# Kernel tuning notes

Hardware: AMD Instinct MI355X
Metric: run time of the kernel (lower is better)

## Reference

```python
import jax, jax.numpy as jnp
import numpy as np

EMBED = 1024

def setup_inputs() -> dict:
    key = jax.random.key(0)
    ks = jax.random.split(key, 10)
    B, S, E = 4, 2048, EMBED
    inv = 1.0 / np.sqrt(E)
    return {
        "query": jax.random.normal(ks[0], (B, S, E), jnp.float32),
        "key": jax.random.normal(ks[1], (B, S, E), jnp.float32),
        "value": jax.random.normal(ks[2], (B, S, E), jnp.float32),
        "attn_mask": jnp.zeros((B, S, S), jnp.float32),
        "Wq": jax.random.normal(ks[3], (E, E), jnp.float32) * inv,
        "bq": jnp.zeros((E,), jnp.float32),
        "Wk": jax.random.normal(ks[4], (E, E), jnp.float32) * inv,
        "bk": jnp.zeros((E,), jnp.float32),
        "Wv": jax.random.normal(ks[5], (E, E), jnp.float32) * inv,
        "bv": jnp.zeros((E,), jnp.float32),
    }

def reference(query, key, value, attn_mask, Wq, bq, Wk, bk, Wv, bv):
    E = query.shape[-1]
    q = query @ Wq.T + bq            # [B,S,E]
    k = key @ Wk.T + bk              # [B,S,E]
    v = value @ Wv.T + bv            # [B,S,E]
    scores = jnp.einsum('bse,bte->bst', q, k) / jnp.sqrt(jnp.float32(E))
    scores = scores + attn_mask      # [B,S,S]
    attn = jax.nn.softmax(scores, axis=-1)
    return jnp.einsum('bst,bte->bse', attn, v)
```

## Files before the change

kernel.cpp:

```cpp
#include <hip/hip_runtime.h>
#include <cstdint>
#include <cstddef>

typedef __bf16 bf16;
typedef __bf16 bf16x8 __attribute__((ext_vector_type(8)));
typedef float  f32x4  __attribute__((ext_vector_type(4)));

#define NB 4
#define SS 2048
#define EE 1024

#define BUFB      49152
#define LDS_TOTAL (3 * BUFB)

static __device__ __forceinline__ void glds16(const bf16* g, void* l)
{
    __builtin_amdgcn_global_load_lds(
        (const __attribute__((address_space(1))) unsigned int*)g,
        (__attribute__((address_space(3))) unsigned int*)l,
        16, 0, 0);
}

static __device__ __forceinline__ void swz_block(int& bx, int& by, int& bz)
{
    const int nx = gridDim.x, ny = gridDim.y;
    const int nwg = nx * ny * gridDim.z;
    int lin = blockIdx.x + nx * (blockIdx.y + ny * blockIdx.z);
    const int per = nwg >> 3;
    lin = (lin & 7) * per + (lin >> 3);
    bz = lin / (nx * ny);
    const int r = lin - bz * nx * ny;
    by = r / nx;
    bx = r - by * nx;
}

static __device__ __forceinline__ void kloop(
    const bf16* __restrict__ A, const bf16* __restrict__ Bm,
    int lda, int ldb, int nt, char* lds, int m0, int n0, int tid,
    f32x4 acc[4][4])
{
    const int lane = tid & 63, w = tid >> 6;
    const int wm = w >> 2, wn = w & 3;
    const int lr = lane & 15, kq = lane >> 4;
    const int axor = (lr & 7) << 4;

    const int srow   = tid >> 3;
    const int chunkL = (tid & 7) ^ (srow & 7);
    const bf16* Asrc = A  + (size_t)(m0 + srow) * lda + chunkL * 8;
    const bf16* Bsrc = Bm + (size_t)(n0 + srow) * ldb + chunkL * 8;
    const int wofs = w << 10;

#pragma unroll
    for (int p = 0; p < 2; ++p) {
        char* d = lds + p * BUFB + wofs;
        const int kt = p * 64;
        glds16(Asrc + kt,                        d);
        glds16(Asrc + (size_t)64 * lda + kt,     d + 8192);
        glds16(Bsrc + kt,                        d + 16384);
        glds16(Bsrc + (size_t)64 * ldb + kt,     d + 16384 + 8192);
        glds16(Bsrc + (size_t)128 * ldb + kt,    d + 16384 + 16384);
        glds16(Bsrc + (size_t)192 * ldb + kt,    d + 16384 + 24576);
    }
    asm volatile("s_waitcnt vmcnt(6)" ::: "memory");
    __builtin_amdgcn_sched_barrier(0);
    __builtin_amdgcn_s_barrier();
    __builtin_amdgcn_sched_barrier(0);

    for (int t = 0; t < nt; ++t) {
        char* la = lds + (t % 3) * BUFB;
        char* lb = la + 16384;
        char* sa = lds + ((t + 2) % 3) * BUFB;
        const bool st = (t + 2) < nt;
        const int kt = (t + 2) * 64;

        bf16x8 af[4], bg[4];
        {
            const int cb = (kq * 16) ^ axor;
#pragma unroll
            for (int m = 0; m < 4; ++m)
                af[m] = *(const bf16x8*)(la + (wm * 64 + m * 16 + lr) * 128 + cb);
#pragma unroll
            for (int n = 0; n < 4; ++n)
                bg[n] = *(const bf16x8*)(lb + (wn * 64 + n * 16 + lr) * 128 + cb);
            if (st) {
                glds16(Asrc + kt,                    sa + wofs);
                glds16(Asrc + (size_t)64 * lda + kt, sa + 8192 + wofs);
                glds16(Bsrc + kt,                    sa + 16384 + wofs);
            }
            __builtin_amdgcn_s_setprio(1);
#pragma unroll
            for (int m = 0; m < 4; ++m)
#pragma unroll
                for (int n = 0; n < 4; ++n)
                    acc[m][n] = __builtin_amdgcn_mfma_f32_16x16x32_bf16(af[m], bg[n], acc[m][n], 0, 0, 0);
            __builtin_amdgcn_s_setprio(0);
        }
        {
            const int cb = (64 + kq * 16) ^ axor;
#pragma unroll
            for (int m = 0; m < 4; ++m)
                af[m] = *(const bf16x8*)(la + (wm * 64 + m * 16 + lr) * 128 + cb);
#pragma unroll
            for (int n = 0; n < 4; ++n)
                bg[n] = *(const bf16x8*)(lb + (wn * 64 + n * 16 + lr) * 128 + cb);
            if (st) {
                glds16(Bsrc + (size_t)64 * ldb + kt,  sa + 16384 + 8192 + wofs);
                glds16(Bsrc + (size_t)128 * ldb + kt, sa + 16384 + 16384 + wofs);
                glds16(Bsrc + (size_t)192 * ldb + kt, sa + 16384 + 24576 + wofs);
            }
            __builtin_amdgcn_s_setprio(1);
#pragma unroll
            for (int m = 0; m < 4; ++m)
#pragma unroll
                for (int n = 0; n < 4; ++n)
                    acc[m][n] = __builtin_amdgcn_mfma_f32_16x16x32_bf16(af[m], bg[n], acc[m][n], 0, 0, 0);
            __builtin_amdgcn_s_setprio(0);
        }
        if (t < nt - 1) {
            if (st) { asm volatile("s_waitcnt vmcnt(6)" ::: "memory"); }
            else    { asm volatile("s_waitcnt vmcnt(0)" ::: "memory"); }
            __builtin_amdgcn_sched_barrier(0);
            __builtin_amdgcn_s_barrier();
            __builtin_amdgcn_sched_barrier(0);
        }
    }
}

__global__ __launch_bounds__(256) void cvt3_kernel(
    const float* __restrict__ s0, const float* __restrict__ s1, const float* __restrict__ s2,
    bf16* __restrict__ d0, bf16* __restrict__ d1, bf16* __restrict__ d2, unsigned n)
{
    const float* s; bf16* d;
    if (blockIdx.y == 0)      { s = s0; d = d0; }
    else if (blockIdx.y == 1) { s = s1; d = d1; }
    else                      { s = s2; d = d2; }
    const size_t i = ((size_t)blockIdx.x * 256 + threadIdx.x) * 8;
    if (i >= n) return;
    const float4 f0 = *(const float4*)(s + i);
    const float4 f1 = *(const float4*)(s + i + 4);
    bf16x8 h;
    h[0] = (bf16)f0.x; h[1] = (bf16)f0.y; h[2] = (bf16)f0.z; h[3] = (bf16)f0.w;
    h[4] = (bf16)f1.x; h[5] = (bf16)f1.y; h[6] = (bf16)f1.z; h[7] = (bf16)f1.w;
    *(bf16x8*)(d + i) = h;
}

__global__ __launch_bounds__(512) void proj8(
    const bf16* __restrict__ qc, const bf16* __restrict__ kc, const bf16* __restrict__ vc,
    const bf16* __restrict__ Wc,
    const float* __restrict__ bq, const float* __restrict__ bk, const float* __restrict__ bv,
    bf16* __restrict__ qb, bf16* __restrict__ kb, bf16* __restrict__ vb)
{
    extern __shared__ char lds[];
    int bx, by, bz; swz_block(bx, by, bz);
    const bf16* A; const float* bias; bf16* out;
    if (bz == 0)      { A = qc; bias = bq; out = qb; }
    else if (bz == 1) { A = kc; bias = bk; out = kb; }
    else              { A = vc; bias = bv; out = vb; }
    const bf16* Bm = Wc + (size_t)bz * EE * EE;

    const int m0 = by * 128, n0 = bx * 256;
    const int tid = threadIdx.x;

    f32x4 acc[4][4];
#pragma unroll
    for (int m = 0; m < 4; ++m)
#pragma unroll
        for (int n = 0; n < 4; ++n) { acc[m][n][0] = 0.f; acc[m][n][1] = 0.f; acc[m][n][2] = 0.f; acc[m][n][3] = 0.f; }

    kloop(A, Bm, EE, EE, EE / 64, lds, m0, n0, tid, acc);

    const int lane = tid & 63, w = tid >> 6, wm = w >> 2, wn = w & 3;
    const int lr = lane & 15, kq = lane >> 4;
#pragma unroll
    for (int n = 0; n < 4; ++n) {
        const int gcol = n0 + wn * 64 + n * 16 + lr;
        const float bb = bias[gcol];
#pragma unroll
        for (int m = 0; m < 4; ++m)
#pragma unroll
            for (int j = 0; j < 4; ++j) {
                const int grow = m0 + wm * 64 + m * 16 + kq * 4 + j;
                out[(size_t)grow * EE + gcol] = (bf16)(acc[m][n][j] + bb);
            }
    }
}

__global__ __launch_bounds__(256) void transpose_kernel(const bf16* __restrict__ vb,
                                                        bf16* __restrict__ vt)
{
    __shared__ bf16 t[64][72];
    const int b  = blockIdx.z;
    const int s0 = blockIdx.x * 64, e0 = blockIdx.y * 64;
    const int tid = threadIdx.x;

    const bf16* src = vb + ((size_t)b * SS + s0) * EE + e0;
#pragma unroll
    for (int i = 0; i < 2; ++i) {
        const int c  = tid * 2 + i;
        const int r  = c >> 3;
        const int cc = (c & 7) * 8;
        *(uint4*)&t[r][cc] = *(const uint4*)&src[(size_t)r * EE + cc];
    }
    __syncthreads();

    bf16* dst = vt + ((size_t)b * EE + e0) * SS + s0;
    const int er  = tid >> 2;
    const int sc0 = (tid & 3) * 16;
    bf16 tmp[16];
#pragma unroll
    for (int k2 = 0; k2 < 16; ++k2) tmp[k2] = t[sc0 + k2][er];
    *(uint4*)&dst[(size_t)er * SS + sc0]     = *(uint4*)&tmp[0];
    *(uint4*)&dst[(size_t)er * SS + sc0 + 8] = *(uint4*)&tmp[8];
}

__global__ __launch_bounds__(512) void scores8(const bf16* __restrict__ qb,
                                               const bf16* __restrict__ kb,
                                               const float* __restrict__ mask,
                                               bf16* __restrict__ sc)
{
    extern __shared__ char lds[];
    int bx, by, bz; swz_block(bx, by, bz);
    const bf16* A  = qb + (size_t)bz * SS * EE;
    const bf16* Bm = kb + (size_t)bz * SS * EE;

    const int m0 = by * 128, n0 = bx * 256;
    const int tid = threadIdx.x;

    f32x4 acc[4][4];
#pragma unroll
    for (int m = 0; m < 4; ++m)
#pragma unroll
        for (int n = 0; n < 4; ++n) { acc[m][n][0] = 0.f; acc[m][n][1] = 0.f; acc[m][n][2] = 0.f; acc[m][n][3] = 0.f; }

    kloop(A, Bm, EE, EE, EE / 64, lds, m0, n0, tid, acc);

    const int lane = tid & 63, w = tid >> 6, wm = w >> 2, wn = w & 3;
    const int lr = lane & 15, kq = lane >> 4;
    const float* mrow = mask + (size_t)bz * SS * SS;
    bf16* out = sc + (size_t)bz * SS * SS;
    const float scale = 0.03125f;
#pragma unroll
    for (int m = 0; m < 4; ++m)
#pragma unroll
        for (int n = 0; n < 4; ++n)
#pragma unroll
            for (int j = 0; j < 4; ++j) {
                const int grow = m0 + wm * 64 + m * 16 + kq * 4 + j;
                const int gcol = n0 + wn * 64 + n * 16 + lr;
                const float v = acc[m][n][j] * scale + mrow[(size_t)grow * SS + gcol];
                out[(size_t)grow * SS + gcol] = (bf16)v;
            }
}

__global__ __launch_bounds__(256) void softmax_kernel(bf16* __restrict__ sc)
{
    __shared__ float red[4];
    const size_t row = blockIdx.x;
    uint4* rp = (uint4*)(sc + row * (size_t)SS);
    const int tid = threadIdx.x, lane = tid & 63, wid = tid >> 6;

    const uint4 d = rp[tid];
    const unsigned int u[4] = { d.x, d.y, d.z, d.w };
    float f[8];
#pragma unroll
    for (int i = 0; i < 4; ++i) {
        union { unsigned int i_; float f_; } lo, hi;
        lo.i_ = u[i] << 16;
        hi.i_ = u[i] & 0xffff0000u;
        f[2 * i]     = lo.f_;
        f[2 * i + 1] = hi.f_;
    }

    float m = f[0];
#pragma unroll
    for (int i = 1; i < 8; ++i) m = fmaxf(m, f[i]);
#pragma unroll
    for (int o = 32; o > 0; o >>= 1) m = fmaxf(m, __shfl_xor(m, o));
    if (lane == 0) red[wid] = m;
    __syncthreads();
    m = fmaxf(fmaxf(red[0], red[1]), fmaxf(red[2], red[3]));
    __syncthreads();

    float e[8], s = 0.f;
#pragma unroll
    for (int i = 0; i < 8; ++i) { e[i] = __expf(f[i] - m); s += e[i]; }
#pragma unroll
    for (int o = 32; o > 0; o >>= 1) s += __shfl_xor(s, o);
    if (lane == 0) red[wid] = s;
    __syncthreads();
    s = red[0] + red[1] + red[2] + red[3];
    const float inv = 1.0f / s;

    unsigned int ou[4];
#pragma unroll
    for (int i = 0; i < 4; ++i) {
        union { bf16 h; unsigned short b; } a0, a1;
        a0.h = (bf16)(e[2 * i] * inv);
        a1.h = (bf16)(e[2 * i + 1] * inv);
        ou[i] = ((unsigned int)a1.b << 16) | (unsigned int)a0.b;
    }
    rp[tid] = make_uint4(ou[0], ou[1], ou[2], ou[3]);
}

__global__ __launch_bounds__(512) void pv8(const bf16* __restrict__ sc,
                                           const bf16* __restrict__ vt,
                                           float* __restrict__ outp)
{
    extern __shared__ char lds[];
    int bx, by, bz; swz_block(bx, by, bz);
    const bf16* A  = sc + (size_t)bz * SS * SS;
    const bf16* Bm = vt + (size_t)bz * EE * SS;

    const int m0 = by * 128, n0 = bx * 256;
    const int tid = threadIdx.x;

    f32x4 acc[4][4];
#pragma unroll
    for (int m = 0; m < 4; ++m)
#pragma unroll
        for (int n = 0; n < 4; ++n) { acc[m][n][0] = 0.f; acc[m][n][1] = 0.f; acc[m][n][2] = 0.f; acc[m][n][3] = 0.f; }

    kloop(A, Bm, SS, SS, SS / 64, lds, m0, n0, tid, acc);

    const int lane = tid & 63, w = tid >> 6, wm = w >> 2, wn = w & 3;
    const int lr = lane & 15, kq = lane >> 4;
#pragma unroll
    for (int m = 0; m < 4; ++m)
#pragma unroll
        for (int n = 0; n < 4; ++n)
#pragma unroll
            for (int j = 0; j < 4; ++j) {
                const int grow = m0 + wm * 64 + m * 16 + kq * 4 + j;
                const int gcol = n0 + wn * 64 + n * 16 + lr;
                outp[((size_t)bz * SS + grow) * EE + gcol] = acc[m][n][j];
            }
}

extern "C" void kernel_launch(void* const* d_in, const int* in_sizes, int n_in,
                              void* d_out, int out_size, void* d_ws, size_t ws_size,
                              hipStream_t stream)
{
    const float* query = (const float*)d_in[0];
    const float* key_  = (const float*)d_in[1];
    const float* value = (const float*)d_in[2];
    const float* mask  = (const float*)d_in[3];
    const float* Wq = (const float*)d_in[4];
    const float* bq = (const float*)d_in[5];
    const float* Wk = (const float*)d_in[6];
    const float* bk = (const float*)d_in[7];
    const float* Wv = (const float*)d_in[8];
    const float* bv = (const float*)d_in[9];
    float* outp = (float*)d_out;

    char* ws = (char*)d_ws;
    const size_t QKV = (size_t)NB * SS * EE * 2;
    const size_t SCB = (size_t)NB * SS * SS * 2;
    const size_t WCB = (size_t)3 * EE * EE * 2;
    if (ws_size < 4 * QKV + SCB + WCB) return;

    bf16* qb = (bf16*)(ws);
    bf16* kb = (bf16*)(ws + QKV);
    bf16* vb = (bf16*)(ws + 2 * QKV);
    bf16* vt = (bf16*)(ws + 3 * QKV);
    bf16* sc = (bf16*)(ws + 4 * QKV);
    bf16* Wc = (bf16*)(ws + 4 * QKV + SCB);
    bf16* qc = vt;
    bf16* kc = sc;
    bf16* vc = (bf16*)(ws + 5 * QKV);

    (void)hipFuncSetAttribute((const void*)proj8,   hipFuncAttributeMaxDynamicSharedMemorySize, LDS_TOTAL);
    (void)hipFuncSetAttribute((const void*)scores8, hipFuncAttributeMaxDynamicSharedMemorySize, LDS_TOTAL);
    (void)hipFuncSetAttribute((const void*)pv8,     hipFuncAttributeMaxDynamicSharedMemorySize, LDS_TOTAL);

    dim3 blk(256), blk5(512);
    const unsigned NQKV = (unsigned)NB * SS * EE;
    const unsigned NW   = (unsigned)EE * EE;
    cvt3_kernel<<<dim3(NQKV / (256 * 8), 3), blk, 0, stream>>>(
        query, key_, value, qc, kc, vc, NQKV);
    cvt3_kernel<<<dim3(NW / (256 * 8), 3), blk, 0, stream>>>(
        Wq, Wk, Wv, Wc, Wc + (size_t)EE * EE, Wc + 2 * (size_t)EE * EE, NW);

    proj8<<<dim3(EE / 256, (NB * SS) / 128, 3), blk5, LDS_TOTAL, stream>>>(
        qc, kc, vc, Wc, bq, bk, bv, qb, kb, vb);
    transpose_kernel<<<dim3(SS / 64, EE / 64, NB), blk, 0, stream>>>(vb, vt);
    scores8<<<dim3(SS / 256, SS / 128, NB), blk5, LDS_TOTAL, stream>>>(qb, kb, mask, sc);
    softmax_kernel<<<dim3(NB * SS), blk, 0, stream>>>(sc);
    pv8<<<dim3(EE / 256, SS / 128, NB), blk5, LDS_TOTAL, stream>>>(sc, vt, outp);
}
```

Before: 196.0 us.

## Halve GEMM K-tile to 32 and deepen LDS pipeline for higher occupancy

The shared GEMM main loop now stages K in steps of 32 instead of 64, using a 24KB per-stage LDS buffer with a 4-chunk XOR swizzle. Projection and scores kernels keep 3 stages and request 4 workgroups per CU. The PV kernel uses a 6-stage ring for deeper prefetch and requests 2 workgroups per CU. The aim is more resident waves and more loads in flight to hide memory latency, at the cost of twice as many barriers per K and possible register pressure from the launch bounds.

```diff
diff --git a/kernel.cpp b/kernel.cpp
--- a/kernel.cpp
+++ b/kernel.cpp
@@ -10,8 +10,9 @@
 #define SS 2048
 #define EE 1024
 
-#define BUFB      49152
-#define LDS_TOTAL (3 * BUFB)
+#define BUFB  24576
+#define LDS3  (3 * BUFB)
+#define LDS6  (6 * BUFB)
 
 static __device__ __forceinline__ void glds16(const bf16* g, void* l)
 {
@@ -34,7 +35,8 @@
     bx = r - by * nx;
 }
 
-static __device__ __forceinline__ void kloop(
+template<int NBUF>
+static __device__ __forceinline__ void kloop32(
     const bf16* __restrict__ A, const bf16* __restrict__ Bm,
     int lda, int ldb, int nt, char* lds, int m0, int n0, int tid,
     f32x4 acc[4][4])
@@ -42,88 +44,67 @@
     const int lane = tid & 63, w = tid >> 6;
     const int wm = w >> 2, wn = w & 3;
     const int lr = lane & 15, kq = lane >> 4;
-    const int axor = (lr & 7) << 4;
-
-    const int srow   = tid >> 3;
-    const int chunkL = (tid & 7) ^ (srow & 7);
+    const int cb = (kq * 16) ^ ((lr & 3) << 4);
+
+    const int srow   = tid >> 2;
+    const int chunkL = (tid & 3) ^ (srow & 3);
     const bf16* Asrc = A  + (size_t)(m0 + srow) * lda + chunkL * 8;
     const bf16* Bsrc = Bm + (size_t)(n0 + srow) * ldb + chunkL * 8;
     const int wofs = w << 10;
 
 #pragma unroll
-    for (int p = 0; p < 2; ++p) {
+    for (int p = 0; p < NBUF - 1; ++p) {
         char* d = lds + p * BUFB + wofs;
-        const int kt = p * 64;
-        glds16(Asrc + kt,                        d);
-        glds16(Asrc + (size_t)64 * lda + kt,     d + 8192);
-        glds16(Bsrc + kt,                        d + 16384);
-        glds16(Bsrc + (size_t)64 * ldb + kt,     d + 16384 + 8192);
-        glds16(Bsrc + (size_t)128 * ldb + kt,    d + 16384 + 16384);
-        glds16(Bsrc + (size_t)192 * ldb + kt,    d + 16384 + 24576);
-    }
-    asm volatile("s_waitcnt vmcnt(6)" ::: "memory");
+        const int kt = p * 32;
+        glds16(Asrc + kt,                     d);
+        glds16(Bsrc + kt,                     d + 8192);
+        glds16(Bsrc + (size_t)128 * ldb + kt, d + 16384);
+    }
+    if constexpr (NBUF == 3) asm volatile("s_waitcnt vmcnt(3)" ::: "memory");
+    else                     asm volatile("s_waitcnt vmcnt(12)" ::: "memory");
     __builtin_amdgcn_sched_barrier(0);
     __builtin_amdgcn_s_barrier();
     __builtin_amdgcn_sched_barrier(0);
 
+    int rb = 0, sb = NBUF - 1;
     for (int t = 0; t < nt; ++t) {
-        char* la = lds + (t % 3) * BUFB;
-        char* lb = la + 16384;
-        char* sa = lds + ((t + 2) % 3) * BUFB;
-        const bool st = (t + 2) < nt;
-        const int kt = (t + 2) * 64;
+        char* la = lds + rb * BUFB;
+        char* lb = la + 8192;
+        const int ts = (t + NBUF - 1 < nt) ? t + NBUF - 1 : nt - 1;
+        const int kt = ts * 32;
+        char* d = lds + sb * BUFB + wofs;
 
         bf16x8 af[4], bg[4];
-        {
-            const int cb = (kq * 16) ^ axor;
-#pragma unroll
-            for (int m = 0; m < 4; ++m)
-                af[m] = *(const bf16x8*)(la + (wm * 64 + m * 16 + lr) * 128 + cb);
+#pragma unroll
+        for (int m = 0; m < 4; ++m)
+            af[m] = *(const bf16x8*)(la + (wm * 64 + m * 16 + lr) * 64 + cb);
+#pragma unroll
+        for (int n = 0; n < 4; ++n)
+            bg[n] = *(const bf16x8*)(lb + (wn * 64 + n * 16 + lr) * 64 + cb);
+
+        glds16(Asrc + kt,                     d);
+        glds16(Bsrc + kt,                     d + 8192);
+        glds16(Bsrc + (size_t)128 * ldb + kt, d + 16384);
+
+        __builtin_amdgcn_s_setprio(1);
+#pragma unroll
+        for (int m = 0; m < 4; ++m)
 #pragma unroll
             for (int n = 0; n < 4; ++n)
-                bg[n] = *(const bf16x8*)(lb + (wn * 64 + n * 16 + lr) * 128 + cb);
-            if (st) {
-                glds16(Asrc + kt,                    sa + wofs);
-                glds16(Asrc + (size_t)64 * lda + kt, sa + 8192 + wofs);
-                glds16(Bsrc + kt,                    sa + 16384 + wofs);
-            }
-            __builtin_amdgcn_s_setprio(1);
-#pragma unroll
-            for (int m = 0; m < 4; ++m)
-#pragma unroll
-                for (int n = 0; n < 4; ++n)
-                    acc[m][n] = __builtin_amdgcn_mfma_f32_16x16x32_bf16(af[m], bg[n], acc[m][n], 0, 0, 0);
-            __builtin_amdgcn_s_setprio(0);
-        }
-        {
-            const int cb = (64 + kq * 16) ^ axor;
-#pragma unroll
-            for (int m = 0; m < 4; ++m)
-                af[m] = *(const bf16x8*)(la + (wm * 64 + m * 16 + lr) * 128 + cb);
-#pragma unroll
-            for (int n = 0; n < 4; ++n)
-                bg[n] = *(const bf16x8*)(lb + (wn * 64 + n * 16 + lr) * 128 + cb);
-            if (st) {
-                glds16(Bsrc + (size_t)64 * ldb + kt,  sa + 16384 + 8192 + wofs);
-                glds16(Bsrc + (size_t)128 * ldb + kt, sa + 16384 + 16384 + wofs);
-                glds16(Bsrc + (size_t)192 * ldb + kt, sa + 16384 + 24576 + wofs);
-            }
-            __builtin_amdgcn_s_setprio(1);
-#pragma unroll
-            for (int m = 0; m < 4; ++m)
-#pragma unroll
-                for (int n = 0; n < 4; ++n)
-                    acc[m][n] = __builtin_amdgcn_mfma_f32_16x16x32_bf16(af[m], bg[n], acc[m][n], 0, 0, 0);
-            __builtin_amdgcn_s_setprio(0);
-        }
+                acc[m][n] = __builtin_amdgcn_mfma_f32_16x16x32_bf16(af[m], bg[n], acc[m][n], 0, 0, 0);
+        __builtin_amdgcn_s_setprio(0);
+
         if (t < nt - 1) {
-            if (st) { asm volatile("s_waitcnt vmcnt(6)" ::: "memory"); }
-            else    { asm volatile("s_waitcnt vmcnt(0)" ::: "memory"); }
+            if constexpr (NBUF == 3) asm volatile("s_waitcnt vmcnt(3)" ::: "memory");
+            else                     asm volatile("s_waitcnt vmcnt(12)" ::: "memory");
             __builtin_amdgcn_sched_barrier(0);
             __builtin_amdgcn_s_barrier();
             __builtin_amdgcn_sched_barrier(0);
         }
-    }
+        rb = (rb + 1 == NBUF) ? 0 : rb + 1;
+        sb = (sb + 1 == NBUF) ? 0 : sb + 1;
+    }
+    asm volatile("s_waitcnt vmcnt(0)" ::: "memory");
 }
 
 __global__ __launch_bounds__(256) void cvt3_kernel(
@@ -144,7 +125,7 @@
     *(bf16x8*)(d + i) = h;
 }
 
-__global__ __launch_bounds__(512) void proj8(
+__global__ __launch_bounds__(512, 4) void proj8(
     const bf16* __restrict__ qc, const bf16* __restrict__ kc, const bf16* __restrict__ vc,
     const bf16* __restrict__ Wc,
     const float* __restrict__ bq, const float* __restrict__ bk, const float* __restrict__ bv,
@@ -167,7 +148,7 @@
 #pragma unroll
         for (int n = 0; n < 4; ++n) { acc[m][n][0] = 0.f; acc[m][n][1] = 0.f; acc[m][n][2] = 0.f; acc[m][n][3] = 0.f; }
 
-    kloop(A, Bm, EE, EE, EE / 64, lds, m0, n0, tid, acc);
+    kloop32<3>(A, Bm, EE, EE, EE / 32, lds, m0, n0, tid, acc);
 
     const int lane = tid & 63, w = tid >> 6, wm = w >> 2, wn = w & 3;
     const int lr = lane & 15, kq = lane >> 4;
@@ -213,10 +194,10 @@
     *(uint4*)&dst[(size_t)er * SS + sc0 + 8] = *(uint4*)&tmp[8];
 }
 
-__global__ __launch_bounds__(512) void scores8(const bf16* __restrict__ qb,
-                                               const bf16* __restrict__ kb,
-                                               const float* __restrict__ mask,
-                                               bf16* __restrict__ sc)
+__global__ __launch_bounds__(512, 4) void scores8(const bf16* __restrict__ qb,
+                                                  const bf16* __restrict__ kb,
+                                                  const float* __restrict__ mask,
+                                                  bf16* __restrict__ sc)
 {
     extern __shared__ char lds[];
     int bx, by, bz; swz_block(bx, by, bz);
@@ -232,7 +213,7 @@
 #pragma unroll
         for (int n = 0; n < 4; ++n) { acc[m][n][0] = 0.f; acc[m][n][1] = 0.f; acc[m][n][2] = 0.f; acc[m][n][3] = 0.f; }
 
-    kloop(A, Bm, EE, EE, EE / 64, lds, m0, n0, tid, acc);
+    kloop32<3>(A, Bm, EE, EE, EE / 32, lds, m0, n0, tid, acc);
 
     const int lane = tid & 63, w = tid >> 6, wm = w >> 2, wn = w & 3;
     const int lr = lane & 15, kq = lane >> 4;
@@ -302,9 +283,9 @@
     rp[tid] = make_uint4(ou[0], ou[1], ou[2], ou[3]);
 }
 
-__global__ __launch_bounds__(512) void pv8(const bf16* __restrict__ sc,
-                                           const bf16* __restrict__ vt,
-                                           float* __restrict__ outp)
+__global__ __launch_bounds__(512, 2) void pv8(const bf16* __restrict__ sc,
+                                              const bf16* __restrict__ vt,
+                                              float* __restrict__ outp)
 {
     extern __shared__ char lds[];
     int bx, by, bz; swz_block(bx, by, bz);
@@ -320,7 +301,7 @@
 #pragma unroll
         for (int n = 0; n < 4; ++n) { acc[m][n][0] = 0.f; acc[m][n][1] = 0.f; acc[m][n][2] = 0.f; acc[m][n][3] = 0.f; }
 
-    kloop(A, Bm, SS, SS, SS / 64, lds, m0, n0, tid, acc);
+    kloop32<6>(A, Bm, SS, SS, SS / 32, lds, m0, n0, tid, acc);
 
     const int lane = tid & 63, w = tid >> 6, wm = w >> 2, wn = w & 3;
     const int lr = lane & 15, kq = lane >> 4;
@@ -368,9 +349,9 @@
     bf16* kc = sc;
     bf16* vc = (bf16*)(ws + 5 * QKV);
 
-    (void)hipFuncSetAttribute((const void*)proj8,   hipFuncAttributeMaxDynamicSharedMemorySize, LDS_TOTAL);
-    (void)hipFuncSetAttribute((const void*)scores8, hipFuncAttributeMaxDynamicSharedMemorySize, LDS_TOTAL);
-    (void)hipFuncSetAttribute((const void*)pv8,     hipFuncAttributeMaxDynamicSharedMemorySize, LDS_TOTAL);
+    (void)hipFuncSetAttribute((const void*)proj8,   hipFuncAttributeMaxDynamicSharedMemorySize, LDS3);
+    (void)hipFuncSetAttribute((const void*)scores8, hipFuncAttributeMaxDynamicSharedMemorySize, LDS3);
+    (void)hipFuncSetAttribute((const void*)pv8,     hipFuncAttributeMaxDynamicSharedMemorySize, LDS6);
 
     dim3 blk(256), blk5(512);
     const unsigned NQKV = (unsigned)NB * SS * EE;
@@ -380,10 +361,10 @@
     cvt3_kernel<<<dim3(NW / (256 * 8), 3), blk, 0, stream>>>(
         Wq, Wk, Wv, Wc, Wc + (size_t)EE * EE, Wc + 2 * (size_t)EE * EE, NW);
 
-    proj8<<<dim3(EE / 256, (NB * SS) / 128, 3), blk5, LDS_TOTAL, stream>>>(
+    proj8<<<dim3(EE / 256, (NB * SS) / 128, 3), blk5, LDS3, stream>>>(
         qc, kc, vc, Wc, bq, bk, bv, qb, kb, vb);
     transpose_kernel<<<dim3(SS / 64, EE / 64, NB), blk, 0, stream>>>(vb, vt);
-    scores8<<<dim3(SS / 256, SS / 128, NB), blk5, LDS_TOTAL, stream>>>(qb, kb, mask, sc);
+    scores8<<<dim3(SS / 256, SS / 128, NB), blk5, LDS3, stream>>>(qb, kb, mask, sc);
     softmax_kernel<<<dim3(NB * SS), blk, 0, stream>>>(sc);
-    pv8<<<dim3(EE / 256, SS / 128, NB), blk5, LDS_TOTAL, stream>>>(sc, vt, outp);
-}
+    pv8<<<dim3(EE / 256, SS / 128, NB), blk5, LDS6, stream>>>(sc, vt, outp);
+}
```

New measurement: 203.6 us. 1.04x slower.
